# Optimization experiments

Measured on AMD Instinct MI355X. Metric: run time of the kernel, lower is better.

## Reference

```python
import jax, jax.numpy as jnp
import numpy as np

SEQ_LEN = 256
FILTER_NUM = 230
BATCH = 2048
NEG_INF = jnp.float32(-1e30)


def setup_inputs() -> dict:
    key = jax.random.key(0)
    k1, k2, k3 = jax.random.split(key, 3)
    conv_output = jax.random.normal(k1, (BATCH, SEQ_LEN, FILTER_NUM), dtype=jnp.float32)
    # positions: e1 = positions[:,1], e2 = positions[:,3]; require 1 <= e1 < e2 <= seq_len-1
    e1 = jax.random.randint(k2, (BATCH,), 1, SEQ_LEN - 2)             # in [1, seq_len-3]
    e2 = e1 + 1 + jax.random.randint(k3, (BATCH,), 0, SEQ_LEN - 1) % (SEQ_LEN - 1 - e1)
    positions = jnp.stack([jnp.zeros_like(e1), e1, e1, e2], axis=1).astype(jnp.int32)
    return {"conv_output": conv_output, "positions": positions}


def reference(conv_output, positions):
    # conv_output: [B, S, F]; positions: [B, 4] int; output: [B, 3F]
    e1 = positions[:, 1][:, None]  # [B, 1]
    e2 = positions[:, 3][:, None]  # [B, 1]
    idx = jnp.arange(SEQ_LEN)[None, :]  # [1, S]
    m1 = (idx < e1)[:, :, None]                 # piece [0, e1)
    m2 = ((idx >= e1) & (idx < e2))[:, :, None]  # piece [e1, e2)
    m3 = (idx >= e2)[:, :, None]                # piece [e2, S)
    p1 = jnp.max(jnp.where(m1, conv_output, NEG_INF), axis=1)  # [B, F]
    p2 = jnp.max(jnp.where(m2, conv_output, NEG_INF), axis=1)
    p3 = jnp.max(jnp.where(m3, conv_output, NEG_INF), axis=1)
    return jnp.concatenate([p1, p2, p3], axis=1)  # [B, 3F]
```

## Files before the change

kernel.cpp:

```cpp
#include <hip/hip_runtime.h>


constexpr int S    = 256;
constexpr int Fn   = 230;
constexpr int HALF = 115;
constexpr float NEG = -1e30f;

__global__ __launch_bounds__(256) void pmax_kernel(
    const float* __restrict__ conv,
    const int*   __restrict__ pos,
    float*       __restrict__ out)
{
    const int b   = blockIdx.x;
    const int tid = threadIdx.x;
    const int e1  = pos[b * 4 + 1];
    const int e2  = pos[b * 4 + 3];
    const float* base = conv + (size_t)b * (S * Fn);

    const bool active = tid < 2 * HALF;
    const int  row    = (tid >= HALF) ? 1 : 0;
    const int  col    = tid - row * HALF;

    float m0x = NEG, m0y = NEG;
    float m1x = NEG, m1y = NEG;
    float m2x = NEG, m2y = NEG;

    if (active) {
        const float* p = base + 2 * col + (size_t)row * Fn;
        const int a1 = e1 - row;
        const int a2 = e2 - row;

        #pragma unroll 8
        for (int sb = 0; sb < S; sb += 2) {
            const float2 v = *(const float2*)(p + (size_t)sb * Fn);
            const bool c1 = sb < a1;
            const bool c2 = sb < a2;
            float t0x = c1 ? v.x : NEG, t0y = c1 ? v.y : NEG;
            float t1x = c2 ? v.x : NEG, t1y = c2 ? v.y : NEG;
            t1x = c1 ? NEG : t1x;       t1y = c1 ? NEG : t1y;
            float t2x = c2 ? NEG : v.x, t2y = c2 ? NEG : v.y;
            m0x = fmaxf(m0x, t0x); m0y = fmaxf(m0y, t0y);
            m1x = fmaxf(m1x, t1x); m1y = fmaxf(m1y, t1y);
            m2x = fmaxf(m2x, t2x); m2y = fmaxf(m2y, t2y);
        }
    }

    __shared__ float red[6][HALF];
    if (active && row) {
        red[0][col] = m0x; red[1][col] = m0y;
        red[2][col] = m1x; red[3][col] = m1y;
        red[4][col] = m2x; red[5][col] = m2y;
    }
    __syncthreads();
    if (active && !row) {
        m0x = fmaxf(m0x, red[0][col]); m0y = fmaxf(m0y, red[1][col]);
        m1x = fmaxf(m1x, red[2][col]); m1y = fmaxf(m1y, red[3][col]);
        m2x = fmaxf(m2x, red[4][col]); m2y = fmaxf(m2y, red[5][col]);

        float* ob = out + (size_t)b * (3 * Fn);
        *(float2*)(ob + 0 * Fn + 2 * col) = make_float2(m0x, m0y);
        *(float2*)(ob + 1 * Fn + 2 * col) = make_float2(m1x, m1y);
        *(float2*)(ob + 2 * Fn + 2 * col) = make_float2(m2x, m2y);
    }
}

extern "C" void kernel_launch(void* const* d_in, const int* in_sizes, int n_in,
                              void* d_out, int out_size, void* d_ws, size_t ws_size,
                              hipStream_t stream)
{
    const float* conv = (const float*)d_in[0];
    const int*   pos  = (const int*)d_in[1];
    float*       out  = (float*)d_out;

    const int B = in_sizes[0] / (S * Fn);
    pmax_kernel<<<B, 256, 0, stream>>>(conv, pos, out);
}
```

Baseline: 91.50 us.

## Use 16-byte nontemporal loads over 4-row chunks with LDS cross-row reduction

Each thread now reads a contiguous float4 from a flattened chunk of 4 rows (920 floats), so 230 threads cover four sequence rows per iteration instead of two rows with float2 loads. Per-lane row offsets adjust the piece boundaries, and a shared-memory pass folds the four row partials into the final per-filter maxima. Loads and stores use nontemporal hints. The intent is wider memory transactions and fewer loop iterations on this bandwidth-bound kernel, at the cost of more registers and a larger LDS reduction.

```diff
diff --git a/kernel.cpp b/kernel.cpp
--- a/kernel.cpp
+++ b/kernel.cpp
@@ -1,66 +1,79 @@
 #include <hip/hip_runtime.h>
 
 
-constexpr int S    = 256;
-constexpr int Fn   = 230;
-constexpr int HALF = 115;
+constexpr int S   = 256;
+constexpr int Fn  = 230;
+constexpr int RPC = 4;
+constexpr int CF  = Fn * RPC;
+constexpr int NCH = S / RPC;
+constexpr int NT  = CF / 4;
 constexpr float NEG = -1e30f;
+
+typedef float f32x4 __attribute__((ext_vector_type(4)));
 
 __global__ __launch_bounds__(256) void pmax_kernel(
     const float* __restrict__ conv,
     const int*   __restrict__ pos,
     float*       __restrict__ out)
 {
-    const int b   = blockIdx.x;
-    const int tid = threadIdx.x;
-    const int e1  = pos[b * 4 + 1];
-    const int e2  = pos[b * 4 + 3];
+    const int b = blockIdx.x;
+    const int t = threadIdx.x;
+    const int e1 = pos[b * 4 + 1];
+    const int e2 = pos[b * 4 + 3];
     const float* base = conv + (size_t)b * (S * Fn);
 
-    const bool active = tid < 2 * HALF;
-    const int  row    = (tid >= HALF) ? 1 : 0;
-    const int  col    = tid - row * HALF;
+    float m[3][4];
+    #pragma unroll
+    for (int p = 0; p < 3; ++p)
+        #pragma unroll
+        for (int j = 0; j < 4; ++j) m[p][j] = NEG;
 
-    float m0x = NEG, m0y = NEG;
-    float m1x = NEG, m1y = NEG;
-    float m2x = NEG, m2y = NEG;
+    if (t < NT) {
+        int a1[4], a2[4];
+        #pragma unroll
+        for (int j = 0; j < 4; ++j) {
+            const int rj = (4 * t + j) / Fn;
+            a1[j] = e1 - rj;
+            a2[j] = e2 - rj;
+        }
+        const float* p0 = base + 4 * t;
 
-    if (active) {
-        const float* p = base + 2 * col + (size_t)row * Fn;
-        const int a1 = e1 - row;
-        const int a2 = e2 - row;
-
-        #pragma unroll 8
-        for (int sb = 0; sb < S; sb += 2) {
-            const float2 v = *(const float2*)(p + (size_t)sb * Fn);
-            const bool c1 = sb < a1;
-            const bool c2 = sb < a2;
-            float t0x = c1 ? v.x : NEG, t0y = c1 ? v.y : NEG;
-            float t1x = c2 ? v.x : NEG, t1y = c2 ? v.y : NEG;
-            t1x = c1 ? NEG : t1x;       t1y = c1 ? NEG : t1y;
-            float t2x = c2 ? NEG : v.x, t2y = c2 ? NEG : v.y;
-            m0x = fmaxf(m0x, t0x); m0y = fmaxf(m0y, t0y);
-            m1x = fmaxf(m1x, t1x); m1y = fmaxf(m1y, t1y);
-            m2x = fmaxf(m2x, t2x); m2y = fmaxf(m2y, t2y);
+        #pragma unroll 4
+        for (int g = 0; g < NCH; ++g) {
+            const f32x4 v = __builtin_nontemporal_load(
+                (const f32x4*)(p0 + (size_t)g * CF));
+            const int s4 = 4 * g;
+            #pragma unroll
+            for (int j = 0; j < 4; ++j) {
+                const float vj = v[j];
+                const bool c1 = s4 < a1[j];
+                const bool c2 = s4 < a2[j];
+                m[0][j] = fmaxf(m[0][j], c1 ? vj : NEG);
+                m[1][j] = fmaxf(m[1][j], c2 ? (c1 ? NEG : vj) : NEG);
+                m[2][j] = fmaxf(m[2][j], c2 ? NEG : vj);
+            }
         }
     }
 
-    __shared__ float red[6][HALF];
-    if (active && row) {
-        red[0][col] = m0x; red[1][col] = m0y;
-        red[2][col] = m1x; red[3][col] = m1y;
-        red[4][col] = m2x; red[5][col] = m2y;
+    __shared__ float lds[3][CF];
+    if (t < NT) {
+        #pragma unroll
+        for (int p = 0; p < 3; ++p) {
+            lds[p][4 * t + 0] = m[p][0];
+            lds[p][4 * t + 1] = m[p][1];
+            lds[p][4 * t + 2] = m[p][2];
+            lds[p][4 * t + 3] = m[p][3];
+        }
     }
     __syncthreads();
-    if (active && !row) {
-        m0x = fmaxf(m0x, red[0][col]); m0y = fmaxf(m0y, red[1][col]);
-        m1x = fmaxf(m1x, red[2][col]); m1y = fmaxf(m1y, red[3][col]);
-        m2x = fmaxf(m2x, red[4][col]); m2y = fmaxf(m2y, red[5][col]);
-
+    if (t < Fn) {
         float* ob = out + (size_t)b * (3 * Fn);
-        *(float2*)(ob + 0 * Fn + 2 * col) = make_float2(m0x, m0y);
-        *(float2*)(ob + 1 * Fn + 2 * col) = make_float2(m1x, m1y);
-        *(float2*)(ob + 2 * Fn + 2 * col) = make_float2(m2x, m2y);
+        #pragma unroll
+        for (int p = 0; p < 3; ++p) {
+            const float mm = fmaxf(fmaxf(lds[p][t],          lds[p][t + Fn]),
+                                   fmaxf(lds[p][t + 2 * Fn], lds[p][t + 3 * Fn]));
+            __builtin_nontemporal_store(mm, ob + p * Fn + t);
+        }
     }
 }
 
```

Measured after the change: 81.75 us, median of 2. 1.12x faster.
